# Kernel optimization log

Hardware: AMD Instinct MI355X
Metric: run time of the kernel (lower is better)

The kernel has to match this reference:

```python
import jax, jax.numpy as jnp
import numpy as np

HIDDEN = 512
HEADS = 8
HEAD_DIM = HIDDEN // HEADS


def setup_inputs() -> dict:
    key = jax.random.key(0)
    ks = jax.random.split(key, 7)
    B, C, H, W = 8, HIDDEN, 32, 32
    scale = 1.0 / np.sqrt(C)
    inputs = jax.random.normal(ks[0], (B, C, H, W), dtype=jnp.float32)
    # 1x1 conv == per-pixel linear; store weights as [C_in, C_out]
    wq = jax.random.normal(ks[1], (C, HIDDEN), dtype=jnp.float32) * scale
    wk = jax.random.normal(ks[2], (C, HIDDEN), dtype=jnp.float32) * scale
    wv = jax.random.normal(ks[3], (C, HIDDEN), dtype=jnp.float32) * scale
    bq = jax.random.normal(ks[4], (HIDDEN,), dtype=jnp.float32) * 0.01
    bk = jax.random.normal(ks[5], (HIDDEN,), dtype=jnp.float32) * 0.01
    bv = jax.random.normal(ks[6], (HIDDEN,), dtype=jnp.float32) * 0.01
    return {"inputs": inputs, "wq": wq, "bq": bq, "wk": wk, "bk": bk, "wv": wv, "bv": bv}


def _proj_heads(x, w, b):
    # x: [B,C,H,W] -> tokens [B,heads,N,head_dim], matching transpose_for_scores
    B, C, H, W = x.shape
    t = jnp.einsum('bchw,cd->bhwd', x, w) + b          # [B,H,W,HIDDEN]
    t = t.reshape(B, H * W, HEADS, HEAD_DIM)
    return t.transpose(0, 2, 1, 3)                      # [B,heads,N,hd]


def reference(inputs, wq, bq, wk, bk, wv, bv):
    B, C, H, W = inputs.shape
    q = _proj_heads(inputs, wq, bq)
    k = _proj_heads(inputs, wk, bk)
    v = _proj_heads(inputs, wv, bv)
    # NOTE: original module applies NO 1/sqrt(d) scaling
    scores = jnp.einsum('bhnd,bhmd->bhnm', q, k)        # [B,heads,N,N]
    probs = jax.nn.softmax(scores, axis=-1)
    ctx = jnp.einsum('bhnm,bhmd->bhnd', probs, v)       # [B,heads,N,hd]
    # [B,heads,N,hd] -> [B,N,heads*hd] -> [B,H,W,C] -> [B,C,H,W]
    out = ctx.transpose(0, 2, 1, 3).reshape(B, H, W, HEADS * HEAD_DIM)
    return out.transpose(0, 3, 1, 2)
```

## Files before the change

kernel.cpp:

```cpp
#include <hip/hip_runtime.h>
#include <hip/hip_bf16.h>
#include <cmath>

#define B_     8
#define C_     512
#define N_     1024
#define HEADS_ 8
#define HD_    64
#define INST_  64

typedef short     v8s __attribute__((ext_vector_type(8)));
typedef _Float16  v8h __attribute__((ext_vector_type(8)));
typedef float    v16f __attribute__((ext_vector_type(16)));
typedef unsigned short ushort_t;
typedef unsigned int   uint_t;

__device__ inline ushort_t f2h(float x) {
    _Float16 h = (_Float16)x;
    ushort_t r; __builtin_memcpy(&r, &h, 2); return r;
}
__device__ inline uint_t pkbf(float a, float b) {
    __hip_bfloat162 p = __float22bfloat162_rn(make_float2(a, b));
    uint_t r; __builtin_memcpy(&r, &p, 4); return r;
}

__global__ __launch_bounds__(256) void prep_kernel(
    const float* __restrict__ x,
    const float* __restrict__ wq, const float* __restrict__ wk,
    const float* __restrict__ wv,
    uint_t* __restrict__ wt, uint_t* __restrict__ xt)
{
    __shared__ uint_t LH[64 * 32];
    const int z = blockIdx.z;
    const float* src;
    int srcStride;
    size_t outRow0;
    uint_t* oh;
    if (z < 3) {
        if (blockIdx.x >= 8) return;
        src = (z == 0) ? wq : (z == 1) ? wk : wv;
        srcStride = 512;
        outRow0 = (size_t)z * 512 + blockIdx.x * 64;
        oh = wt;
    } else {
        int b = z - 3;
        src = x + (size_t)b * C_ * N_;
        srcStride = 1024;
        outRow0 = (size_t)b * 1024 + blockIdx.x * 64;
        oh = xt;
    }
    const int d0 = blockIdx.x * 64;
    const int c0 = blockIdx.y * 64;
    const int t  = threadIdx.x;

    #pragma unroll
    for (int rep = 0; rep < 2; ++rep) {
        int idx = rep * 256 + t;
        int cp  = idx >> 4;
        int dq  = idx & 15;
        float4 fa = *(const float4*)&src[(size_t)(c0 + 2 * cp) * srcStride + d0 + dq * 4];
        float4 fb = *(const float4*)&src[(size_t)(c0 + 2 * cp + 1) * srcStride + d0 + dq * 4];
        float aa[4] = {fa.x, fa.y, fa.z, fa.w};
        float bb[4] = {fb.x, fb.y, fb.z, fb.w};
        #pragma unroll
        for (int j = 0; j < 4; ++j) {
            int d_l = dq * 4 + j;
            LH[d_l * 32 + (cp ^ (d_l & 31))] =
                (uint_t)f2h(aa[j]) | ((uint_t)f2h(bb[j]) << 16);
        }
    }
    __syncthreads();

    const int d_l = t >> 2;
    const int wq4 = (t & 3) * 8;
    uint_t vh[8];
    #pragma unroll
    for (int i = 0; i < 8; ++i)
        vh[i] = LH[d_l * 32 + ((wq4 + i) ^ (d_l & 31))];
    size_t base = (outRow0 + d_l) * 256 + c0 / 2 + wq4;
    *(uint4*)&oh[base]     = *(uint4*)&vh[0];
    *(uint4*)&oh[base + 4] = *(uint4*)&vh[4];
}

__global__ __launch_bounds__(256) void proj_kernel(
    const _Float16* __restrict__ xt, const _Float16* __restrict__ wt,
    const float* __restrict__ bq, const float* __restrict__ bk,
    const float* __restrict__ bv,
    ushort_t* __restrict__ qf, ushort_t* __restrict__ kf,
    ushort_t* __restrict__ vt)
{
    __shared__ _Float16 POOL[12288];

    const int tok0  = blockIdx.x * 64;
    const int b     = tok0 >> 10;
    const int ntb   = tok0 & 1023;
    const int by    = blockIdx.y;
    const int which = by >> 2;
    const int nloc0 = (by & 3) * 128;

    const int t   = threadIdx.x;
    const int w   = t >> 6;
    const int l   = t & 63;
    const int l31 = l & 31;
    const int h5  = l >> 5;
    const int wm  = w & 1;
    const int wn  = w >> 1;

    const int g   = t & 3;
    const int r0  = t >> 2;
    const int swz = g ^ (r0 & 3);

    const _Float16* baseA = xt + (size_t)(tok0 + r0) * 512 + g * 8;
    const _Float16* baseB = wt + (size_t)(which * 512 + nloc0 + r0) * 512 + g * 8;

    v8h pfa, pfb0, pfb1;
    auto load_tile = [&](int k0) {
        pfa  = *(const v8h*)(baseA + k0);
        pfb0 = *(const v8h*)(baseB + k0);
        pfb1 = *(const v8h*)(baseB + 32768 + k0);
    };
    auto store_tile = [&](int off) {
        *(v8h*)&POOL[off + (r0 * 4 + swz) * 8] = pfa;
        *(v8h*)&POOL[off + 2048 + (r0 * 4 + swz) * 8] = pfb0;
        int row = 64 + r0;
        *(v8h*)&POOL[off + 2048 + (row * 4 + (g ^ (row & 3))) * 8] = pfb1;
    };

    v16f acc[2] = {{}, {}};

    load_tile(0);
    store_tile(0);
    __syncthreads();

    for (int step = 0; step < 16; ++step) {
        const int off  = (step & 1) ? 6144 : 0;
        const int offn = (step & 1) ? 0 : 6144;
        if (step < 15) load_tile((step + 1) * 32);

        #pragma unroll
        for (int kc = 0; kc < 2; ++kc) {
            int rm = wm * 32 + l31;
            v8h af = *(const v8h*)&POOL[off + (rm * 4 + ((kc * 2 + h5) ^ (rm & 3))) * 8];
            v8h bf[2];
            #pragma unroll
            for (int ns = 0; ns < 2; ++ns) {
                int rn = wn * 64 + ns * 32 + l31;
                bf[ns] = *(const v8h*)&POOL[off + 2048 +
                          (rn * 4 + ((kc * 2 + h5) ^ (rn & 3))) * 8];
            }
            #pragma unroll
            for (int ns = 0; ns < 2; ++ns)
                acc[ns] = __builtin_amdgcn_mfma_f32_32x32x16_f16(
                    af, bf[ns], acc[ns], 0, 0, 0);
        }

        if (step < 15) {
            store_tile(offn);
            __syncthreads();
        }
    }

    if (which < 2) {
        ushort_t* oh = (which == 0) ? qf : kf;
        const float* bias = (which == 0) ? bq : bk;
        #pragma unroll
        for (int ns = 0; ns < 2; ++ns) {
            int d_local = nloc0 + wn * 64 + ns * 32 + l31;
            float bvv  = bias[d_local];
            int head   = d_local >> 6;
            int hd     = d_local & 63;
            size_t pb  = (size_t)(b * HEADS_ + head) * 65536 + hd;
            #pragma unroll
            for (int r = 0; r < 16; ++r) {
                int n = ntb + wm * 32 + (r & 3) + 8 * (r >> 2) + 4 * h5;
                oh[pb + (size_t)n * 64] = f2h(acc[ns][r] + bvv);
            }
        }
    } else {
        float bvv[2];
        #pragma unroll
        for (int ns = 0; ns < 2; ++ns)
            bvv[ns] = bv[nloc0 + wn * 64 + ns * 32 + l31];
        __syncthreads();
        uint_t* TW = (uint_t*)POOL + w * 1024;
        #pragma unroll
        for (int ns = 0; ns < 2; ++ns)
            #pragma unroll
            for (int r = 0; r < 16; r += 2) {
                int tok_l = (r & 3) + 8 * (r >> 2) + 4 * h5;
                int hd_l  = ns * 32 + l31;
                TW[hd_l * 16 + ((tok_l >> 1) ^ (hd_l & 15))] =
                    pkbf(acc[ns][r] + bvv[ns], acc[ns][r + 1] + bvv[ns]);
            }
        __syncthreads();
        const int head = (nloc0 + wn * 64) >> 6;
        uint_t* vtu = (uint_t*)vt;
        size_t base = (size_t)(b * HEADS_ + head) * 32768 + (size_t)l * 512
                    + (ntb + wm * 32) / 2;
        #pragma unroll
        for (int c = 0; c < 4; ++c) {
            uint_t wd[4];
            #pragma unroll
            for (int kk = 0; kk < 4; ++kk) {
                int wsx = c * 4 + kk;
                int w3 = wsx & 7;
                int sw = (wsx & ~7) | (w3 & 1) | (((w3 >> 1) & 1) << 2)
                                   | (((w3 >> 2) & 1) << 1);
                wd[kk] = TW[l * 16 + (sw ^ (l & 15))];
            }
            *(uint4*)&vtu[base + c * 4] = *(uint4*)&wd[0];
        }
    }
}

__global__ __launch_bounds__(256) void attn_kernel(
    const ushort_t* __restrict__ qf, const ushort_t* __restrict__ kf,
    const ushort_t* __restrict__ vt, float* __restrict__ out)
{
    __shared__ _Float16 KH[8192];
    __shared__ ushort_t VT[8192];
    __shared__ float    RS[128];

    const int inst  = blockIdx.x;
    const int chunk = blockIdx.y;
    const int t     = threadIdx.x;
    const int w     = t >> 6;
    const int l     = t & 63;
    const int l31   = l & 31;
    const int h5    = l >> 5;

    const ushort_t* Qf = qf + (size_t)inst * 65536;
    const ushort_t* Kf = kf + (size_t)inst * 65536;
    const ushort_t* Vt = vt + (size_t)inst * 65536;

    const int qbase = chunk * 128 + w * 32;

    v8h aq[4];
    #pragma unroll
    for (int ks = 0; ks < 4; ++ks)
        aq[ks] = *(const v8h*)&Qf[(size_t)(qbase + l31) * 64 + ks * 16 + h5 * 8];

    const int g   = t & 7;
    const int r0  = t >> 3;
    const int swz = g ^ (r0 & 7);
    const ushort_t* baseK = Kf + (size_t)r0 * 64 + g * 8;
    const ushort_t* baseV = Vt + (size_t)r0 * 1024 + g * 8;

    v8h pk0, pk1; v8s pv0, pv1;
    auto load_tile = [&](int kt) {
        pk0 = *(const v8h*)(baseK + (size_t)kt * 4096);
        pk1 = *(const v8h*)(baseK + (size_t)kt * 4096 + 2048);
        pv0 = *(const v8s*)(baseV + (size_t)kt * 64);
        pv1 = *(const v8s*)(baseV + 32768 + (size_t)kt * 64);
    };
    auto store_tile = [&](int off) {
        int so0 = (r0 * 8 + swz) * 8;
        int so1 = ((32 + r0) * 8 + swz) * 8;
        *(v8h*)&KH[off + so0] = pk0;
        *(v8h*)&KH[off + so1] = pk1;
        *(v8s*)&VT[off + so0] = pv0;
        *(v8s*)&VT[off + so1] = pv1;
    };

    v16f O0 = {}, O1 = {};
    float rsumv = 0.f;

    load_tile(0);
    store_tile(0);
    __syncthreads();

    for (int kt = 0; kt < 16; ++kt) {
        const int off  = (kt & 1) ? 4096 : 0;
        const int offn = (kt & 1) ? 0 : 4096;
        if (kt < 15) load_tile(kt + 1);

        #pragma unroll
        for (int t2 = 0; t2 < 2; ++t2) {
            v16f s = {};
            int kvrow = t2 * 32 + l31;
            #pragma unroll
            for (int ks = 0; ks < 4; ++ks) {
                int so = (kvrow * 8 + ((ks * 2 + h5) ^ (kvrow & 7))) * 8;
                v8h khf = *(const v8h*)&KH[off + so];
                s = __builtin_amdgcn_mfma_f32_32x32x16_f16(khf, aq[ks], s, 0, 0, 0);
            }
            float e0[8], e1[8];
            #pragma unroll
            for (int j = 0; j < 8; ++j) {
                e0[j] = __expf(s[j] - 64.0f);
                e1[j] = __expf(s[8 + j] - 64.0f);
                rsumv += e0[j] + e1[j];
            }
            uint4 u0, u1;
            u0.x = pkbf(e0[0], e0[1]); u0.y = pkbf(e0[2], e0[3]);
            u0.z = pkbf(e0[4], e0[5]); u0.w = pkbf(e0[6], e0[7]);
            u1.x = pkbf(e1[0], e1[1]); u1.y = pkbf(e1[2], e1[3]);
            u1.z = pkbf(e1[4], e1[5]); u1.w = pkbf(e1[6], e1[7]);
            v8s p0 = __builtin_bit_cast(v8s, u0);
            v8s p1 = __builtin_bit_cast(v8s, u1);

            #pragma unroll
            for (int hh = 0; hh < 2; ++hh) {
                int rv = hh * 32 + l31;
                int g0 = (4 * t2 + h5)     ^ (rv & 7);
                int g1 = (4 * t2 + 2 + h5) ^ (rv & 7);
                v8s bv0 = *(const v8s*)&VT[off + (rv * 8 + g0) * 8];
                v8s bv1 = *(const v8s*)&VT[off + (rv * 8 + g1) * 8];
                if (hh == 0) {
                    O0 = __builtin_amdgcn_mfma_f32_32x32x16_bf16(p0, bv0, O0, 0, 0, 0);
                    O0 = __builtin_amdgcn_mfma_f32_32x32x16_bf16(p1, bv1, O0, 0, 0, 0);
                } else {
                    O1 = __builtin_amdgcn_mfma_f32_32x32x16_bf16(p0, bv0, O1, 0, 0, 0);
                    O1 = __builtin_amdgcn_mfma_f32_32x32x16_bf16(p1, bv1, O1, 0, 0, 0);
                }
            }
        }

        if (kt < 15) {
            store_tile(offn);
            __syncthreads();
        }
    }

    float tot = rsumv + __shfl_xor(rsumv, 32, 64);
    if (h5 == 0) RS[w * 32 + l31] = 1.0f / tot;
    __syncthreads();
    float invr[16];
    #pragma unroll
    for (int r = 0; r < 16; ++r)
        invr[r] = RS[w * 32 + (r & 3) + 8 * (r >> 2) + 4 * h5];

    const int b    = inst >> 3;
    const int head = inst & 7;
    float* ob = out + (size_t)b * C_ * N_;
    #pragma unroll
    for (int hh = 0; hh < 2; ++hh) {
        const v16f& O = hh ? O1 : O0;
        int c = head * 64 + hh * 32 + l31;
        #pragma unroll
        for (int qd = 0; qd < 4; ++qd) {
            int n = qbase + 8 * qd + 4 * h5;
            float4 o4;
            o4.x = O[qd * 4 + 0] * invr[qd * 4 + 0];
            o4.y = O[qd * 4 + 1] * invr[qd * 4 + 1];
            o4.z = O[qd * 4 + 2] * invr[qd * 4 + 2];
            o4.w = O[qd * 4 + 3] * invr[qd * 4 + 3];
            *(float4*)&ob[(size_t)c * N_ + n] = o4;
        }
    }
}

extern "C" void kernel_launch(void* const* d_in, const int* in_sizes, int n_in,
                              void* d_out, int out_size, void* d_ws, size_t ws_size,
                              hipStream_t stream) {
    const float* x  = (const float*)d_in[0];
    const float* wq = (const float*)d_in[1];
    const float* bq = (const float*)d_in[2];
    const float* wk = (const float*)d_in[3];
    const float* bk = (const float*)d_in[4];
    const float* wv = (const float*)d_in[5];
    const float* bv = (const float*)d_in[6];
    float* out = (float*)d_out;

    char* ws = (char*)d_ws;
    _Float16* wt = (_Float16*)(ws);
    _Float16* xt = (_Float16*)(ws + 1572864);
    ushort_t* qf = (ushort_t*)(ws + 9961472);
    ushort_t* kf = (ushort_t*)(ws + 18350080);
    ushort_t* vt = (ushort_t*)(ws + 26738688);

    prep_kernel<<<dim3(16, 8, 11), 256, 0, stream>>>(
        x, wq, wk, wv, (uint_t*)wt, (uint_t*)xt);
    proj_kernel<<<dim3(128, 12), 256, 0, stream>>>(xt, wt, bq, bk, bv,
                                                   qf, kf, vt);
    attn_kernel<<<dim3(64, 8), 256, 0, stream>>>(qf, kf, vt, out);
}
```

Baseline: 143.0 us.

## Split attention over key halves and add a combine kernel

The attention kernel now splits the 1024 keys into two halves along a new grid dimension, doubling the number of blocks. Each block writes unnormalised partial outputs and row sums to workspace, and a new combine kernel sums the halves, normalises and writes the final layout. The aim is more parallelism and occupancy across CUs, at the cost of extra global memory traffic for partials and an additional kernel launch.

```diff
diff --git a/kernel.cpp b/kernel.cpp
--- a/kernel.cpp
+++ b/kernel.cpp
@@ -215,14 +215,15 @@
 
 __global__ __launch_bounds__(256) void attn_kernel(
     const ushort_t* __restrict__ qf, const ushort_t* __restrict__ kf,
-    const ushort_t* __restrict__ vt, float* __restrict__ out)
+    const ushort_t* __restrict__ vt,
+    float* __restrict__ opart, float* __restrict__ rsp)
 {
     __shared__ _Float16 KH[8192];
     __shared__ ushort_t VT[8192];
-    __shared__ float    RS[128];
 
     const int inst  = blockIdx.x;
     const int chunk = blockIdx.y;
+    const int z     = blockIdx.z;
     const int t     = threadIdx.x;
     const int w     = t >> 6;
     const int l     = t & 63;
@@ -243,8 +244,8 @@
     const int g   = t & 7;
     const int r0  = t >> 3;
     const int swz = g ^ (r0 & 7);
-    const ushort_t* baseK = Kf + (size_t)r0 * 64 + g * 8;
-    const ushort_t* baseV = Vt + (size_t)r0 * 1024 + g * 8;
+    const ushort_t* baseK = Kf + (size_t)(z * 512 + r0) * 64 + g * 8;
+    const ushort_t* baseV = Vt + (size_t)r0 * 1024 + z * 512 + g * 8;
 
     v8h pk0, pk1; v8s pv0, pv1;
     auto load_tile = [&](int kt) {
@@ -269,10 +270,10 @@
     store_tile(0);
     __syncthreads();
 
-    for (int kt = 0; kt < 16; ++kt) {
+    for (int kt = 0; kt < 8; ++kt) {
         const int off  = (kt & 1) ? 4096 : 0;
         const int offn = (kt & 1) ? 0 : 4096;
-        if (kt < 15) load_tile(kt + 1);
+        if (kt < 7) load_tile(kt + 1);
 
         #pragma unroll
         for (int t2 = 0; t2 < 2; ++t2) {
@@ -316,35 +317,79 @@
             }
         }
 
-        if (kt < 15) {
+        if (kt < 7) {
             store_tile(offn);
             __syncthreads();
         }
     }
 
+    const size_t blk = (size_t)(z * 512 + inst * 8 + chunk);
     float tot = rsumv + __shfl_xor(rsumv, 32, 64);
-    if (h5 == 0) RS[w * 32 + l31] = 1.0f / tot;
+    if (h5 == 0)
+        rsp[blk * 128 + w * 32 + l31] = tot;
+
+    float* ob = opart + (blk * 256 + t) * 32;
+    #pragma unroll
+    for (int hh = 0; hh < 2; ++hh) {
+        const v16f& O = hh ? O1 : O0;
+        #pragma unroll
+        for (int qd = 0; qd < 4; ++qd) {
+            float4 o4;
+            o4.x = O[qd * 4 + 0];
+            o4.y = O[qd * 4 + 1];
+            o4.z = O[qd * 4 + 2];
+            o4.w = O[qd * 4 + 3];
+            *(float4*)&ob[hh * 16 + qd * 4] = o4;
+        }
+    }
+}
+
+__global__ __launch_bounds__(256) void combine_kernel(
+    const float* __restrict__ opart, const float* __restrict__ rsp,
+    float* __restrict__ out)
+{
+    __shared__ float RS[128];
+    const int inst  = blockIdx.x;
+    const int chunk = blockIdx.y;
+    const int t     = threadIdx.x;
+    const int w     = t >> 6;
+    const int l     = t & 63;
+    const int l31   = l & 31;
+    const int h5    = l >> 5;
+
+    const size_t i0 = (size_t)(inst * 8 + chunk);
+    const size_t i1 = i0 + 512;
+
+    if (h5 == 0) {
+        int q = w * 32 + l31;
+        RS[q] = 1.0f / (rsp[i0 * 128 + q] + rsp[i1 * 128 + q]);
+    }
     __syncthreads();
     float invr[16];
     #pragma unroll
     for (int r = 0; r < 16; ++r)
         invr[r] = RS[w * 32 + (r & 3) + 8 * (r >> 2) + 4 * h5];
 
+    const float* p0 = opart + (i0 * 256 + t) * 32;
+    const float* p1 = opart + (i1 * 256 + t) * 32;
+
     const int b    = inst >> 3;
     const int head = inst & 7;
+    const int qbase = chunk * 128 + w * 32;
     float* ob = out + (size_t)b * C_ * N_;
     #pragma unroll
     for (int hh = 0; hh < 2; ++hh) {
-        const v16f& O = hh ? O1 : O0;
         int c = head * 64 + hh * 32 + l31;
         #pragma unroll
         for (int qd = 0; qd < 4; ++qd) {
+            float4 a = *(const float4*)&p0[hh * 16 + qd * 4];
+            float4 bb = *(const float4*)&p1[hh * 16 + qd * 4];
             int n = qbase + 8 * qd + 4 * h5;
             float4 o4;
-            o4.x = O[qd * 4 + 0] * invr[qd * 4 + 0];
-            o4.y = O[qd * 4 + 1] * invr[qd * 4 + 1];
-            o4.z = O[qd * 4 + 2] * invr[qd * 4 + 2];
-            o4.w = O[qd * 4 + 3] * invr[qd * 4 + 3];
+            o4.x = (a.x + bb.x) * invr[qd * 4 + 0];
+            o4.y = (a.y + bb.y) * invr[qd * 4 + 1];
+            o4.z = (a.z + bb.z) * invr[qd * 4 + 2];
+            o4.w = (a.w + bb.w) * invr[qd * 4 + 3];
             *(float4*)&ob[(size_t)c * N_ + n] = o4;
         }
     }
@@ -368,10 +413,13 @@
     ushort_t* qf = (ushort_t*)(ws + 9961472);
     ushort_t* kf = (ushort_t*)(ws + 18350080);
     ushort_t* vt = (ushort_t*)(ws + 26738688);
+    float*  opart = (float*)(ws + 35127296);
+    float*  rsp   = (float*)(ws + 68681728);
 
     prep_kernel<<<dim3(16, 8, 11), 256, 0, stream>>>(
         x, wq, wk, wv, (uint_t*)wt, (uint_t*)xt);
     proj_kernel<<<dim3(128, 12), 256, 0, stream>>>(xt, wt, bq, bk, bv,
                                                    qf, kf, vt);
-    attn_kernel<<<dim3(64, 8), 256, 0, stream>>>(qf, kf, vt, out);
-}
+    attn_kernel<<<dim3(64, 8, 2), 256, 0, stream>>>(qf, kf, vt, opart, rsp);
+    combine_kernel<<<dim3(64, 8), 256, 0, stream>>>(opart, rsp, out);
+}
```

Measured after the change: 160.6 us. 12.3% more time.
